# Kernel tuning notes

Hardware: AMD Instinct MI355X
Metric: run time of the kernel (lower is better)

The kernel has to match this reference:

```python
import jax, jax.numpy as jnp
import numpy as np

B = 8      # number of drug-target pairs in the packed batch
NR = 3200  # total packed residues
NA = 320   # total packed atoms
TD = 512   # target (GearNet) feature dim
DD = 128   # drug (EGNN) feature dim
H = 128    # hidden_dim


def setup_inputs() -> dict:
    key = jax.random.key(0)
    ks = jax.random.split(key, 10)
    seg_res = jnp.sort(jax.random.randint(ks[0], (NR,), 0, B, dtype=jnp.int32))
    seg_atom = jnp.sort(jax.random.randint(ks[1], (NA,), 0, B, dtype=jnp.int32))
    return {
        "target_feature": jax.random.normal(ks[2], (NR, TD), jnp.float32),
        "drug_feature": jax.random.normal(ks[3], (NA, DD), jnp.float32),
        "target_pos": jax.random.normal(ks[4], (NR, 3), jnp.float32) * 10.0,
        "drug_pos": jax.random.normal(ks[5], (NA, 3), jnp.float32) * 10.0,
        "Wt": jax.random.normal(ks[6], (TD, H), jnp.float32) / np.sqrt(TD).astype(np.float32),
        "bt": jnp.zeros((H,), jnp.float32),
        "Wd": jax.random.normal(ks[7], (DD, H), jnp.float32) / np.sqrt(DD).astype(np.float32),
        "bd": jnp.zeros((H,), jnp.float32),
        "seg_res": seg_res,
        "seg_atom": seg_atom,
    }


def reference(target_feature, drug_feature, target_pos, drug_pos, Wt, bt, Wd, bd, seg_res, seg_atom):
    # Linear projections (torchdrug MLP with a single hidden dim == plain Linear)
    tf = target_feature @ Wt + bt  # [NR, H]
    df = drug_feature @ Wd + bd    # [NA, H]

    # Block-diagonal mask: pair (i, j) is valid iff residue i and atom j belong
    # to the same DT-pair (replaces the Python loop that zeroes cross blocks).
    mask = seg_res[:, None] == seg_atom[None, :]  # [NR, NA]

    # Pairwise residue-atom distances
    D = jnp.linalg.norm(target_pos[:, None, :] - drug_pos[None, :, :], axis=-1)  # [NR, NA]

    # Per-block min/max distance (min/max over the masked block only)
    row_min = jnp.min(jnp.where(mask, D, jnp.inf), axis=1)   # [NR]
    row_max = jnp.max(jnp.where(mask, D, -jnp.inf), axis=1)  # [NR]
    dmin = jax.ops.segment_min(row_min, seg_res, num_segments=B)  # [B]
    dmax = jax.ops.segment_max(row_max, seg_res, num_segments=B)  # [B]
    dmin = jnp.where(jnp.isfinite(dmin), dmin, 0.0)
    dmax = jnp.where(jnp.isfinite(dmax), dmax, 1.0)
    denom = jnp.where(dmax > dmin, dmax - dmin, 1.0)

    # Normalized distance inside blocks, zero outside (matches the torch loop)
    dnorm = jnp.where(mask, (D - dmin[seg_res][:, None]) / denom[seg_res][:, None], 0.0)

    # Feature difference inside blocks, zero outside
    imap = jnp.where(mask[:, :, None], tf[:, None, :] - df[None, :, :], 0.0)  # [NR, NA, H]

    # scaled=False -> no 1/sqrt(hidden_dim) scaling
    return jnp.tanh(imap + dnorm[:, :, None])
```

## Files before the change

### kernel.cpp

```cpp
#include <hip/hip_runtime.h>
#include <math.h>

constexpr int NR = 3200;
constexpr int NA = 320;
constexpr int TD = 512;
constexpr int DD = 128;
constexpr int H  = 128;
constexpr int B  = 8;
constexpr int NP = NR * NA;

constexpr int ROWS_T = 4;
constexpr int ROWS_D = 8;
constexpr int NBLK_T = NR / ROWS_T;
constexpr int NBLK_D = NA / ROWS_D;

typedef float f4 __attribute__((ext_vector_type(4)));

__global__ __launch_bounds__(256) void mega_kernel(
    const float* __restrict__ At, const float* __restrict__ Wt, const float* __restrict__ bt,
    const float* __restrict__ Ad, const float* __restrict__ Wd, const float* __restrict__ bd,
    const float* __restrict__ tpos, const float* __restrict__ dpos,
    const int* __restrict__ seg_res, const int* __restrict__ seg_atom,
    float* __restrict__ tf, float* __restrict__ df,
    float* __restrict__ Dbuf, float* __restrict__ rowmin, float* __restrict__ rowmax) {
    __shared__ float sA[ROWS_T * TD];
    __shared__ float sAcc[ROWS_D * H];
    const int b = blockIdx.x;
    const int t = threadIdx.x;

    if (b < NBLK_T) {
        const int h = t & (H - 1), half = t >> 7, i0 = b * ROWS_T;
        for (int idx = t; idx < ROWS_T * TD; idx += 256)
            sA[idx] = At[i0 * TD + idx];
        __syncthreads();
        float acc[ROWS_T];
#pragma unroll
        for (int r = 0; r < ROWS_T; r++) acc[r] = 0.0f;
        const int k0 = half * (TD / 2), k1 = k0 + (TD / 2);
#pragma unroll 4
        for (int k = k0; k < k1; k++) {
            const float w = Wt[k * H + h];
#pragma unroll
            for (int r = 0; r < ROWS_T; r++)
                acc[r] = fmaf(sA[r * TD + k], w, acc[r]);
        }
        if (half) {
#pragma unroll
            for (int r = 0; r < ROWS_T; r++) sAcc[r * H + h] = acc[r];
        }
        __syncthreads();
        if (!half) {
            const float bv = bt[h];
#pragma unroll
            for (int r = 0; r < ROWS_T; r++)
                tf[(i0 + r) * H + h] = acc[r] + sAcc[r * H + h] + bv;
        }
    } else if (b < NBLK_T + NBLK_D) {
        const int h = t & (H - 1), half = t >> 7, i0 = (b - NBLK_T) * ROWS_D;
        for (int idx = t; idx < ROWS_D * DD; idx += 256)
            sA[idx] = Ad[i0 * DD + idx];
        __syncthreads();
        float acc[ROWS_D];
#pragma unroll
        for (int r = 0; r < ROWS_D; r++) acc[r] = 0.0f;
        const int k0 = half * (DD / 2), k1 = k0 + (DD / 2);
#pragma unroll 4
        for (int k = k0; k < k1; k++) {
            const float w = Wd[k * H + h];
#pragma unroll
            for (int r = 0; r < ROWS_D; r++)
                acc[r] = fmaf(sA[r * DD + k], w, acc[r]);
        }
        if (half) {
#pragma unroll
            for (int r = 0; r < ROWS_D; r++) sAcc[r * H + h] = acc[r];
        }
        __syncthreads();
        if (!half) {
            const float bv = bd[h];
#pragma unroll
            for (int r = 0; r < ROWS_D; r++)
                df[(i0 + r) * H + h] = acc[r] + sAcc[r * H + h] + bv;
        }
    } else {
        const int i  = b - NBLK_T - NBLK_D;
        const int sr = seg_res[i];
        const float tx = tpos[3 * i], ty = tpos[3 * i + 1], tz = tpos[3 * i + 2];
        float vmin = INFINITY, vmax = -INFINITY;
        for (int j = t; j < NA; j += 256) {
            const float dx = tx - dpos[3 * j];
            const float dy = ty - dpos[3 * j + 1];
            const float dz = tz - dpos[3 * j + 2];
            const float d  = sqrtf(dx * dx + dy * dy + dz * dz);
            Dbuf[i * NA + j] = d;
            if (seg_atom[j] == sr) {
                vmin = fminf(vmin, d);
                vmax = fmaxf(vmax, d);
            }
        }
#pragma unroll
        for (int off = 32; off > 0; off >>= 1) {
            vmin = fminf(vmin, __shfl_down(vmin, off));
            vmax = fmaxf(vmax, __shfl_down(vmax, off));
        }
        const int wid = t >> 6, lane = t & 63;
        if (lane == 0) { sAcc[wid] = vmin; sAcc[4 + wid] = vmax; }
        __syncthreads();
        if (t == 0) {
            float mn = sAcc[0], mx = sAcc[4];
#pragma unroll
            for (int w = 1; w < 4; w++) {
                mn = fminf(mn, sAcc[w]);
                mx = fmaxf(mx, sAcc[4 + w]);
            }
            rowmin[i] = mn;
            rowmax[i] = mx;
        }
    }
}

__global__ __launch_bounds__(512) void segreduce_kernel(
    const float* __restrict__ rowmin, const float* __restrict__ rowmax,
    const int* __restrict__ seg_res, float2* __restrict__ params) {
    const int s    = threadIdx.x >> 6;
    const int lane = threadIdx.x & 63;
    float mn = INFINITY, mx = -INFINITY;
    for (int r = lane; r < NR; r += 64) {
        if (seg_res[r] == s) {
            mn = fminf(mn, rowmin[r]);
            mx = fmaxf(mx, rowmax[r]);
        }
    }
#pragma unroll
    for (int off = 32; off > 0; off >>= 1) {
        mn = fminf(mn, __shfl_down(mn, off));
        mx = fmaxf(mx, __shfl_down(mx, off));
    }
    if (lane == 0) {
        const float dmin = (mn < INFINITY)  ? mn : 0.0f;
        const float dmax = (mx > -INFINITY) ? mx : 1.0f;
        const float denom = (dmax > dmin) ? (dmax - dmin) : 1.0f;
        params[s] = make_float2(dmin, 1.0f / denom);
    }
}

__device__ __forceinline__ float fast_tanh(float x) {
    const float cx = fminf(fmaxf(x, -15.0f), 15.0f);
    const float e  = __expf(2.0f * cx);
    return 1.0f - __fdividef(2.0f, e + 1.0f);
}

__global__ __launch_bounds__(256) void final_kernel(
    const float* __restrict__ tf, const float* __restrict__ df,
    const float* __restrict__ Dbuf,
    const int* __restrict__ seg_res, const int* __restrict__ seg_atom,
    const float2* __restrict__ params, float* __restrict__ out) {
    const int i = blockIdx.y;
    const int e = (blockIdx.x * 256 + threadIdx.x) * 4;
    const int j = e >> 7;
    const int h = e & 127;

    f4 o = {0.0f, 0.0f, 0.0f, 0.0f};
    const int sr = seg_res[i];
    if (seg_atom[j] == sr) {
        const float2 pp = params[sr];
        const float  dn = (Dbuf[i * NA + j] - pp.x) * pp.y;
        const f4 tv = *(const f4*)(tf + i * H + h);
        const f4 dv = *(const f4*)(df + j * H + h);
        o.x = fast_tanh(tv.x - dv.x + dn);
        o.y = fast_tanh(tv.y - dv.y + dn);
        o.z = fast_tanh(tv.z - dv.z + dn);
        o.w = fast_tanh(tv.w - dv.w + dn);
    }
    __builtin_nontemporal_store(o, (f4*)(out + (long long)i * (NA * H) + e));
}

extern "C" void kernel_launch(void* const* d_in, const int* in_sizes, int n_in,
                              void* d_out, int out_size, void* d_ws, size_t ws_size,
                              hipStream_t stream) {
    const float* target_feature = (const float*)d_in[0];
    const float* drug_feature   = (const float*)d_in[1];
    const float* target_pos     = (const float*)d_in[2];
    const float* drug_pos       = (const float*)d_in[3];
    const float* Wt             = (const float*)d_in[4];
    const float* bt             = (const float*)d_in[5];
    const float* Wd             = (const float*)d_in[6];
    const float* bd             = (const float*)d_in[7];
    const int*   seg_res        = (const int*)d_in[8];
    const int*   seg_atom       = (const int*)d_in[9];
    float* out = (float*)d_out;

    float* ws     = (float*)d_ws;
    float* tf     = ws;
    float* df     = tf + NR * H;
    float* Dbuf   = df + NA * H;
    float* rowmin = Dbuf + NP;
    float* rowmax = rowmin + NR;
    float2* params = (float2*)(rowmax + NR);

    mega_kernel<<<NBLK_T + NBLK_D + NR, 256, 0, stream>>>(
        target_feature, Wt, bt, drug_feature, Wd, bd,
        target_pos, drug_pos, seg_res, seg_atom, tf, df, Dbuf, rowmin, rowmax);
    segreduce_kernel<<<1, 512, 0, stream>>>(rowmin, rowmax, seg_res, params);
    final_kernel<<<dim3(NA * H / (4 * 256), NR), 256, 0, stream>>>(
        tf, df, Dbuf, seg_res, seg_atom, params, out);
}
```

Baseline: 564.7 us.

## Process one residue row per block with shared-memory staging and atom ranges

The final kernel now runs one block per residue row. Each block stages that row's tf vector and its normalized distances in shared memory, then loops over the full output row. The segment reduce kernel also computes the contiguous atom index range of each segment, so the mask test becomes a range check instead of a per-element seg_atom load. This cuts redundant global loads and block-launch overhead in the dominant write-bound kernel, at the cost of fewer blocks and a loop of 40 iterations per thread.

```diff
diff --git a/kernel.cpp b/kernel.cpp
--- a/kernel.cpp
+++ b/kernel.cpp
@@ -121,9 +121,20 @@
 
 __global__ __launch_bounds__(512) void segreduce_kernel(
     const float* __restrict__ rowmin, const float* __restrict__ rowmax,
-    const int* __restrict__ seg_res, float2* __restrict__ params) {
-    const int s    = threadIdx.x >> 6;
-    const int lane = threadIdx.x & 63;
+    const int* __restrict__ seg_res, const int* __restrict__ seg_atom,
+    float2* __restrict__ params, int2* __restrict__ jrange) {
+    __shared__ int sjlo[B], sjhi[B];
+    const int t    = threadIdx.x;
+    const int s    = t >> 6;
+    const int lane = t & 63;
+    if (t < B) { sjlo[t] = NA; sjhi[t] = 0; }
+    __syncthreads();
+    if (t < NA) {
+        const int a = seg_atom[t];
+        atomicMin(&sjlo[a], t);
+        atomicMax(&sjhi[a], t + 1);
+    }
+
     float mn = INFINITY, mx = -INFINITY;
     for (int r = lane; r < NR; r += 64) {
         if (seg_res[r] == s) {
@@ -136,11 +147,13 @@
         mn = fminf(mn, __shfl_down(mn, off));
         mx = fmaxf(mx, __shfl_down(mx, off));
     }
+    __syncthreads();
     if (lane == 0) {
         const float dmin = (mn < INFINITY)  ? mn : 0.0f;
         const float dmax = (mx > -INFINITY) ? mx : 1.0f;
         const float denom = (dmax > dmin) ? (dmax - dmin) : 1.0f;
         params[s] = make_float2(dmin, 1.0f / denom);
+        jrange[s] = make_int2(sjlo[s], sjhi[s]);
     }
 }
 
@@ -153,26 +166,40 @@
 __global__ __launch_bounds__(256) void final_kernel(
     const float* __restrict__ tf, const float* __restrict__ df,
     const float* __restrict__ Dbuf,
-    const int* __restrict__ seg_res, const int* __restrict__ seg_atom,
-    const float2* __restrict__ params, float* __restrict__ out) {
-    const int i = blockIdx.y;
-    const int e = (blockIdx.x * 256 + threadIdx.x) * 4;
-    const int j = e >> 7;
-    const int h = e & 127;
-
-    f4 o = {0.0f, 0.0f, 0.0f, 0.0f};
+    const int* __restrict__ seg_res,
+    const float2* __restrict__ params, const int2* __restrict__ jrange,
+    float* __restrict__ out) {
+    __shared__ f4    stf[H / 4];
+    __shared__ float sdn[NA];
+    const int i = blockIdx.x;
+    const int t = threadIdx.x;
     const int sr = seg_res[i];
-    if (seg_atom[j] == sr) {
-        const float2 pp = params[sr];
-        const float  dn = (Dbuf[i * NA + j] - pp.x) * pp.y;
-        const f4 tv = *(const f4*)(tf + i * H + h);
-        const f4 dv = *(const f4*)(df + j * H + h);
-        o.x = fast_tanh(tv.x - dv.x + dn);
-        o.y = fast_tanh(tv.y - dv.y + dn);
-        o.z = fast_tanh(tv.z - dv.z + dn);
-        o.w = fast_tanh(tv.w - dv.w + dn);
-    }
-    __builtin_nontemporal_store(o, (f4*)(out + (long long)i * (NA * H) + e));
+    const float2 pp = params[sr];
+    const int2   jr = jrange[sr];
+
+    if (t < H / 4) stf[t] = ((const f4*)(tf + i * H))[t];
+    for (int j = t; j < NA; j += 256)
+        sdn[j] = (Dbuf[i * NA + j] - pp.x) * pp.y;
+    __syncthreads();
+
+    float* rowout = out + (long long)i * (NA * H);
+#pragma unroll 2
+    for (int e4 = t; e4 < NA * H / 4; e4 += 256) {
+        const int e = e4 * 4;
+        const int j = e >> 7;
+        const int h = e & 127;
+        f4 o = {0.0f, 0.0f, 0.0f, 0.0f};
+        if (j >= jr.x && j < jr.y) {
+            const float dn = sdn[j];
+            const f4 tv = stf[h >> 2];
+            const f4 dv = *(const f4*)(df + j * H + h);
+            o.x = fast_tanh(tv.x - dv.x + dn);
+            o.y = fast_tanh(tv.y - dv.y + dn);
+            o.z = fast_tanh(tv.z - dv.z + dn);
+            o.w = fast_tanh(tv.w - dv.w + dn);
+        }
+        __builtin_nontemporal_store(o, (f4*)(rowout + e));
+    }
 }
 
 extern "C" void kernel_launch(void* const* d_in, const int* in_sizes, int n_in,
@@ -197,11 +224,12 @@
     float* rowmin = Dbuf + NP;
     float* rowmax = rowmin + NR;
     float2* params = (float2*)(rowmax + NR);
+    int2*   jrange = (int2*)(params + B);
 
     mega_kernel<<<NBLK_T + NBLK_D + NR, 256, 0, stream>>>(
         target_feature, Wt, bt, drug_feature, Wd, bd,
         target_pos, drug_pos, seg_res, seg_atom, tf, df, Dbuf, rowmin, rowmax);
-    segreduce_kernel<<<1, 512, 0, stream>>>(rowmin, rowmax, seg_res, params);
-    final_kernel<<<dim3(NA * H / (4 * 256), NR), 256, 0, stream>>>(
-        tf, df, Dbuf, seg_res, seg_atom, params, out);
-}
+    segreduce_kernel<<<1, 512, 0, stream>>>(rowmin, rowmax, seg_res, seg_atom,
+                                            params, jrange);
+    final_kernel<<<NR, 256, 0, stream>>>(tf, df, Dbuf, seg_res, params, jrange, out);
+}
```

New measurement: 583.1 us. +3.3%, slower.
